# Performance work log

Hardware: AMD Instinct MI355X
Metric: run time of the kernel (lower is better)

Reference implementation:

```python
import jax, jax.numpy as jnp
import numpy as np

N = 100000   # nodes
E = 800000   # edges (avg degree 8)
IN_DIM = 384
HID = 256
BN_EPS = 1e-5


def setup_inputs() -> dict:
    key = jax.random.key(0)
    ks = jax.random.split(key, 12)
    x = jax.random.normal(ks[0], (N, IN_DIM), dtype=jnp.float32)
    edge_index = jax.random.randint(ks[1], (2, E), 0, N, dtype=jnp.int32)
    # GCNConv params (glorot-ish scaling)
    W1 = jax.random.normal(ks[2], (IN_DIM, HID), dtype=jnp.float32) * (1.0 / np.sqrt(IN_DIM))
    b1 = jnp.zeros((HID,), jnp.float32)
    W2 = jax.random.normal(ks[3], (HID, HID), dtype=jnp.float32) * (1.0 / np.sqrt(HID))
    b2 = jnp.zeros((HID,), jnp.float32)
    # BatchNorm affine params
    g1 = jnp.ones((HID,), jnp.float32)
    be1 = jnp.zeros((HID,), jnp.float32)
    g2 = jnp.ones((HID,), jnp.float32)
    be2 = jnp.zeros((HID,), jnp.float32)
    return {"x": x, "edge_index": edge_index, "W1": W1, "b1": b1, "g1": g1,
            "be1": be1, "W2": W2, "b2": b2, "g2": g2, "be2": be2}


def _gcn_conv(x, W, b, src, dst):
    """PyG GCNConv: self-loops + symmetric normalization D^-1/2 A D^-1/2."""
    h = x @ W                                             # [N, H]
    deg = jnp.zeros((x.shape[0],), h.dtype).at[dst].add(1.0) + 1.0  # in-deg + self loop
    dinv = jax.lax.rsqrt(deg)                             # [N]
    coef = dinv[src] * dinv[dst]                          # [E]
    agg = jnp.zeros_like(h).at[dst].add(h[src] * coef[:, None])     # scatter-add messages
    agg = agg + h * (1.0 / deg)[:, None]                  # self-loop term (norm = 1/deg)
    return agg + b


def _batchnorm(h, gamma, beta):
    # training-mode BN over node dim, biased variance (matches torch normalization)
    mu = jnp.mean(h, axis=0)
    var = jnp.mean(jnp.square(h - mu), axis=0)
    return gamma * (h - mu) * jax.lax.rsqrt(var + BN_EPS) + beta


def reference(x, edge_index, W1, b1, g1, be1, W2, b2, g2, be2):
    src, dst = edge_index[0], edge_index[1]
    h = _gcn_conv(x, W1, b1, src, dst)
    h = jax.nn.relu(_batchnorm(h, g1, be1))
    # dropout: eval mode -> identity
    h = _gcn_conv(h, W2, b2, src, dst)
    h = jax.nn.relu(_batchnorm(h, g2, be2))
    return h
```

## Files before the change

kernel.cpp:

```cpp
#include <hip/hip_runtime.h>
#include <hip/hip_bf16.h>

#define NN  100000
#define NE  800000
#define KIN 384
#define HID 256
#define BN_EPS 1e-5f

typedef __attribute__((ext_vector_type(4))) float floatx4;
typedef __attribute__((ext_vector_type(8))) short short8;

__device__ __forceinline__ unsigned short f2b(float f) {
    union { float f; unsigned int u; } v; v.f = f;
    unsigned int r = v.u + 0x7fffu + ((v.u >> 16) & 1u);
    return (unsigned short)(r >> 16);
}
__device__ __forceinline__ float b2f(unsigned short h) {
    union { unsigned int u; float f; } v; v.u = ((unsigned int)h) << 16;
    return v.f;
}

__device__ __forceinline__ void gload_lds16(const void* g, void* l) {
    __builtin_amdgcn_global_load_lds(
        (const __attribute__((address_space(1))) void*)g,
        (__attribute__((address_space(3))) void*)l, 16, 0, 0);
}

__global__ __launch_bounds__(256) void k_prep0(
    const float* __restrict__ W1, unsigned short* __restrict__ W1t,
    const float* __restrict__ W2, unsigned short* __restrict__ W2t,
    const int* __restrict__ dst, int* __restrict__ deg)
{
    const int b = blockIdx.x;
    if (b < KIN) {
        W1t[(size_t)threadIdx.x * KIN + b] = f2b(W1[(size_t)b * HID + threadIdx.x]);
    } else if (b < KIN + HID) {
        const int k2 = b - KIN;
        W2t[(size_t)threadIdx.x * HID + k2] = f2b(W2[(size_t)k2 * HID + threadIdx.x]);
    } else {
        const int i = (b - KIN - HID) * 256 + threadIdx.x;
        if (i < NE) atomicAdd(deg + dst[i], 1);
    }
}

__device__ __forceinline__ int block_incl_scan(int v, int* lds) {
    lds[threadIdx.x] = v; __syncthreads();
    #pragma unroll
    for (int off = 1; off < 256; off <<= 1) {
        int t = lds[threadIdx.x];
        int a = (threadIdx.x >= off) ? lds[threadIdx.x - off] : 0;
        __syncthreads();
        lds[threadIdx.x] = t + a;
        __syncthreads();
    }
    return lds[threadIdx.x];
}

__global__ __launch_bounds__(256) void k_scan1(const int* __restrict__ deg,
                                               int* __restrict__ bsum,
                                               float* __restrict__ dinv) {
    __shared__ int lds[256];
    int i = blockIdx.x * 256 + threadIdx.x;
    int v = (i < NN) ? deg[i] : 0;
    if (i < NN) dinv[i] = rsqrtf((float)(v + 1));
    int incl = block_incl_scan(v, lds);
    if (threadIdx.x == 255) bsum[blockIdx.x] = incl;
}

__global__ __launch_bounds__(512) void k_scan2(const int* __restrict__ bsum,
                                               int* __restrict__ boff, int nb,
                                               int* __restrict__ rowptr) {
    __shared__ int lds[512];
    int v = (threadIdx.x < nb) ? bsum[threadIdx.x] : 0;
    lds[threadIdx.x] = v; __syncthreads();
    #pragma unroll
    for (int off = 1; off < 512; off <<= 1) {
        int t = lds[threadIdx.x];
        int a = (threadIdx.x >= off) ? lds[threadIdx.x - off] : 0;
        __syncthreads();
        lds[threadIdx.x] = t + a;
        __syncthreads();
    }
    if (threadIdx.x < nb) boff[threadIdx.x] = lds[threadIdx.x] - v;
    if (threadIdx.x == 0) rowptr[NN] = NE;
}

__global__ __launch_bounds__(256) void k_scan3(const int* __restrict__ deg,
                                               const int* __restrict__ boff,
                                               int* __restrict__ rowptr) {
    __shared__ int lds[256];
    int i = blockIdx.x * 256 + threadIdx.x;
    int v = (i < NN) ? deg[i] : 0;
    int incl = block_incl_scan(v, lds);
    if (i < NN) rowptr[i] = incl - v + boff[blockIdx.x];
}

__global__ __launch_bounds__(256) void k_fill(
    const int* __restrict__ src, const int* __restrict__ dst,
    const float* __restrict__ dinv, const int* __restrict__ rowptr,
    int* __restrict__ cursor, int2* __restrict__ epk)
{
    int e = blockIdx.x * 256 + threadIdx.x;
    if (e < NE) {
        const int d = dst[e], s = src[e];
        const int pos = rowptr[d] + atomicAdd(cursor + d, 1);
        int2 rec; rec.x = s; rec.y = __float_as_int(dinv[s]);
        epk[pos] = rec;
    }
}

template<int K, int MODE, int ABF16>
__global__ __launch_bounds__(512) void k_gemm(
    const void* __restrict__ Av, const unsigned short* __restrict__ Bt,
    unsigned short* __restrict__ C,
    const float* __restrict__ bnacc, const float* __restrict__ g,
    const float* __restrict__ be, int M)
{
    constexpr int BM = 128, BK = 32, LDA = 40, LDB = 32;
    __shared__ __align__(16) unsigned short As[BM * LDA];
    __shared__ __align__(16) unsigned short Bs[HID * LDB];
    __shared__ float s_sc[HID], s_bi[HID];
    const int tid = threadIdx.x;
    const int lane = tid & 63;
    const int wid  = tid >> 6;
    const int wm = wid & 1, wn = wid >> 1;
    const int l15 = lane & 15, lq = lane >> 4;
    const int row0 = blockIdx.x * BM;

    if (MODE) {
        if (tid < HID) {
            const float inv_n = 1.f / (float)NN;
            const float mu  = bnacc[tid] * inv_n;
            const float var = bnacc[HID + tid] * inv_n - mu * mu;
            const float s   = g[tid] * rsqrtf(var + BN_EPS);
            s_sc[tid] = s;
            s_bi[tid] = be[tid] - s * mu;
        }
        __syncthreads();
    }

    floatx4 acc[4][4] = {};

    const int ar  = tid >> 3;
    const int ak  = (tid & 7) * 4;
    const int ar2 = tid >> 2;
    const int ak2 = (tid & 3) * 8;
    const int lofs = (wid << 11) + lane * 16;
    int brow[2], bcol[2];
    #pragma unroll
    for (int r = 0; r < 2; ++r) {
        const int la = lofs + (r << 10);
        brow[r] = la >> 6;
        bcol[r] = (la & 63) >> 1;
    }

    float4 apf0, apf1;
    short8 apf2 = {};
    if (ABF16) {
        const unsigned short* A = (const unsigned short*)Av;
        const int grow = row0 + ar2;
        if (grow < M) apf2 = *(const short8*)(A + (size_t)grow * K + ak2);
    } else {
        const float* A = (const float*)Av;
        const int g0 = row0 + ar, g1 = row0 + 64 + ar;
        apf0 = (g0 < M) ? *(const float4*)(A + (size_t)g0 * K + ak) : make_float4(0.f,0.f,0.f,0.f);
        apf1 = (g1 < M) ? *(const float4*)(A + (size_t)g1 * K + ak) : make_float4(0.f,0.f,0.f,0.f);
    }

    for (int k0 = 0; k0 < K; k0 += BK) {
        #pragma unroll
        for (int r = 0; r < 2; ++r)
            gload_lds16(Bt + (size_t)brow[r] * K + k0 + bcol[r],
                        (char*)Bs + lofs + (r << 10));

        if (ABF16) {
            float x[8];
            #pragma unroll
            for (int t = 0; t < 8; ++t) x[t] = b2f((unsigned short)apf2[t]);
            if (MODE) {
                float4 s0 = *(const float4*)(s_sc + k0 + ak2);
                float4 s1 = *(const float4*)(s_sc + k0 + ak2 + 4);
                float4 b0 = *(const float4*)(s_bi + k0 + ak2);
                float4 b1 = *(const float4*)(s_bi + k0 + ak2 + 4);
                x[0] = fmaxf(x[0] * s0.x + b0.x, 0.f);
                x[1] = fmaxf(x[1] * s0.y + b0.y, 0.f);
                x[2] = fmaxf(x[2] * s0.z + b0.z, 0.f);
                x[3] = fmaxf(x[3] * s0.w + b0.w, 0.f);
                x[4] = fmaxf(x[4] * s1.x + b1.x, 0.f);
                x[5] = fmaxf(x[5] * s1.y + b1.y, 0.f);
                x[6] = fmaxf(x[6] * s1.z + b1.z, 0.f);
                x[7] = fmaxf(x[7] * s1.w + b1.w, 0.f);
            }
            short8 o;
            #pragma unroll
            for (int t = 0; t < 8; ++t) o[t] = (short)f2b(x[t]);
            *(short8*)(As + ar2 * LDA + ak2) = o;
        } else {
            ushort4 o0, o1;
            o0.x = f2b(apf0.x); o0.y = f2b(apf0.y); o0.z = f2b(apf0.z); o0.w = f2b(apf0.w);
            o1.x = f2b(apf1.x); o1.y = f2b(apf1.y); o1.z = f2b(apf1.z); o1.w = f2b(apf1.w);
            *(ushort4*)(As + ar * LDA + ak) = o0;
            *(ushort4*)(As + (64 + ar) * LDA + ak) = o1;
        }

        const int kn = k0 + BK;
        if (kn < K) {
            if (ABF16) {
                const unsigned short* A = (const unsigned short*)Av;
                const int grow = row0 + ar2;
                apf2 = {};
                if (grow < M) apf2 = *(const short8*)(A + (size_t)grow * K + kn + ak2);
            } else {
                const float* A = (const float*)Av;
                const int g0 = row0 + ar, g1 = row0 + 64 + ar;
                apf0 = (g0 < M) ? *(const float4*)(A + (size_t)g0 * K + kn + ak) : make_float4(0.f,0.f,0.f,0.f);
                apf1 = (g1 < M) ? *(const float4*)(A + (size_t)g1 * K + kn + ak) : make_float4(0.f,0.f,0.f,0.f);
            }
        }

        __syncthreads();

        short8 af[4], bf[4];
        #pragma unroll
        for (int i = 0; i < 4; ++i)
            af[i] = *(const short8*)(As + (wm * 64 + i * 16 + l15) * LDA + lq * 8);
        #pragma unroll
        for (int j = 0; j < 4; ++j)
            bf[j] = *(const short8*)(Bs + (wn * 64 + j * 16 + l15) * LDB + lq * 8);
        #pragma unroll
        for (int i = 0; i < 4; ++i)
            #pragma unroll
            for (int j = 0; j < 4; ++j)
                acc[i][j] = __builtin_amdgcn_mfma_f32_16x16x32_bf16(af[i], bf[j], acc[i][j], 0, 0, 0);
        __syncthreads();
    }

    #pragma unroll
    for (int i = 0; i < 4; ++i) {
        #pragma unroll
        for (int r = 0; r < 4; ++r) {
            const int m = row0 + wm * 64 + i * 16 + lq * 4 + r;
            if (m < M) {
                #pragma unroll
                for (int j = 0; j < 4; ++j) {
                    const int c = wn * 64 + j * 16 + l15;
                    C[(size_t)m * HID + c] = f2b(acc[i][j][r]);
                }
            }
        }
    }
}

__global__ __launch_bounds__(256) void k_gather(
    const unsigned short* __restrict__ H, const int2* __restrict__ epk,
    const int* __restrict__ rowptr, const float* __restrict__ dinv,
    unsigned short* __restrict__ AGGb, float* __restrict__ bn_acc)
{
    __shared__ float ls[512];
    const int tid = threadIdx.x, lane = tid & 63, w = tid >> 6;
    const int half = lane >> 5;
    const int l32  = lane & 31;
    const int c0   = l32 * 8;
    float s[8] = {}, q[8] = {};

    for (int n = blockIdx.x * 4 + w; n < NN; n += gridDim.x * 4) {
        const int beg = rowptr[n], end = rowptr[n + 1];
        const float di = dinv[n];
        float a[8] = {};
        int j = beg;
        for (; j + 8 <= end; j += 8) {
            int2 e[4]; short8 h[4];
            #pragma unroll
            for (int t = 0; t < 4; ++t) e[t] = epk[j + half + 2 * t];
            #pragma unroll
            for (int t = 0; t < 4; ++t)
                h[t] = *(const short8*)(H + (size_t)e[t].x * HID + c0);
            #pragma unroll
            for (int t = 0; t < 4; ++t) {
                const float cf = __int_as_float(e[t].y) * di;
                #pragma unroll
                for (int u = 0; u < 8; ++u)
                    a[u] += b2f((unsigned short)h[t][u]) * cf;
            }
        }
        for (; j + 2 <= end; j += 2) {
            const int2 e = epk[j + half];
            const float cf = __int_as_float(e.y) * di;
            const short8 h = *(const short8*)(H + (size_t)e.x * HID + c0);
            #pragma unroll
            for (int u = 0; u < 8; ++u)
                a[u] += b2f((unsigned short)h[u]) * cf;
        }
        if (j < end && half == 0) {
            const int2 e = epk[j];
            const float cf = __int_as_float(e.y) * di;
            const short8 h = *(const short8*)(H + (size_t)e.x * HID + c0);
            #pragma unroll
            for (int u = 0; u < 8; ++u)
                a[u] += b2f((unsigned short)h[u]) * cf;
        }
        if (half == 1) {
            const float cs = di * di;
            const short8 h = *(const short8*)(H + (size_t)n * HID + c0);
            #pragma unroll
            for (int u = 0; u < 8; ++u)
                a[u] += b2f((unsigned short)h[u]) * cs;
        }
        #pragma unroll
        for (int u = 0; u < 8; ++u)
            a[u] += __shfl_xor(a[u], 32);
        if (half == 0) {
            short8 o;
            #pragma unroll
            for (int u = 0; u < 8; ++u) o[u] = (short)f2b(a[u]);
            *(short8*)(AGGb + (size_t)n * HID + c0) = o;
            #pragma unroll
            for (int u = 0; u < 8; ++u) { s[u] += a[u]; q[u] += a[u] * a[u]; }
        }
    }

    ls[tid] = 0.f; ls[tid + 256] = 0.f;
    __syncthreads();
    if (half == 0) {
        #pragma unroll
        for (int u = 0; u < 8; ++u) {
            atomicAdd(&ls[c0 + u], s[u]);
            atomicAdd(&ls[256 + c0 + u], q[u]);
        }
    }
    __syncthreads();
    atomicAdd(bn_acc + tid, ls[tid]);
    atomicAdd(bn_acc + 256 + tid, ls[tid + 256]);
}

__global__ __launch_bounds__(256) void k_apply(
    const unsigned short* __restrict__ AGGb, const float* __restrict__ bnacc,
    const float* __restrict__ g, const float* __restrict__ be,
    float* __restrict__ out)
{
    const int gid = blockIdx.x * 256 + threadIdx.x;
    if (gid < NN * (HID / 4)) {
        const int c4 = (gid & 63) * 4;
        float sc[4], bi[4];
        const float inv_n = 1.f / (float)NN;
        #pragma unroll
        for (int u = 0; u < 4; ++u) {
            const int c = c4 + u;
            const float mu  = bnacc[c] * inv_n;
            const float var = bnacc[HID + c] * inv_n - mu * mu;
            const float sv  = g[c] * rsqrtf(var + BN_EPS);
            sc[u] = sv; bi[u] = be[c] - sv * mu;
        }
        ushort4 v = *(const ushort4*)(AGGb + (size_t)gid * 4);
        float4 o;
        o.x = fmaxf(b2f(v.x) * sc[0] + bi[0], 0.f);
        o.y = fmaxf(b2f(v.y) * sc[1] + bi[1], 0.f);
        o.z = fmaxf(b2f(v.z) * sc[2] + bi[2], 0.f);
        o.w = fmaxf(b2f(v.w) * sc[3] + bi[3], 0.f);
        *(float4*)(out + (size_t)gid * 4) = o;
    }
}

extern "C" void kernel_launch(void* const* d_in, const int* in_sizes, int n_in,
                              void* d_out, int out_size, void* d_ws, size_t ws_size,
                              hipStream_t stream)
{
    const float* x   = (const float*)d_in[0];
    const int*   ei  = (const int*)d_in[1];
    const float* W1  = (const float*)d_in[2];
    const float* g1  = (const float*)d_in[4];
    const float* be1 = (const float*)d_in[5];
    const float* W2  = (const float*)d_in[6];
    const float* g2  = (const float*)d_in[8];
    const float* be2 = (const float*)d_in[9];
    float* out = (float*)d_out;
    const int* srcp = ei;
    const int* dstp = ei + NE;

    constexpr int NB = (NN + 255) / 256;

    char* p = (char*)d_ws;
    int*            deg    = (int*)p;             p += (size_t)NN * 4;
    int*            cursor = (int*)p;             p += (size_t)NN * 4;
    float*          bn1    = (float*)p;           p += 512 * 4;
    float*          bn2    = (float*)p;           p += 512 * 4;
    const size_t zbytes = (size_t)NN * 8 + 4096;
    unsigned short* AGGb   = (unsigned short*)p;  p += (size_t)NN * HID * 2;
    unsigned short* H      = (unsigned short*)p;  p += (size_t)NN * HID * 2;
    float*          dinv   = (float*)p;           p += (size_t)NN * 4;
    int*            rowptr = (int*)p;             p += (size_t)(NN + 1) * 4;
    int2*           epk    = (int2*)p;            p += (size_t)NE * 8;
    int*            bsum   = (int*)p;             p += 512 * 4;
    int*            boff   = (int*)p;             p += 512 * 4;
    unsigned short* W1t    = (unsigned short*)p;  p += (size_t)KIN * HID * 2;
    unsigned short* W2t    = (unsigned short*)p;  p += (size_t)HID * HID * 2;

    hipMemsetAsync(deg, 0, zbytes, stream);

    k_prep0<<<KIN + HID + (NE + 255) / 256, 256, 0, stream>>>(W1, W1t, W2, W2t, dstp, deg);

    k_scan1<<<NB, 256, 0, stream>>>(deg, bsum, dinv);
    k_scan2<<<1, 512, 0, stream>>>(bsum, boff, NB, rowptr);
    k_scan3<<<NB, 256, 0, stream>>>(deg, boff, rowptr);
    k_fill<<<(NE + 255) / 256, 256, 0, stream>>>(srcp, dstp, dinv, rowptr, cursor, epk);

    const int ggrid = (NN + 127) / 128;

    k_gemm<KIN, 0, 0><<<ggrid, 512, 0, stream>>>(x, W1t, H, nullptr, nullptr, nullptr, NN);
    k_gather<<<2560, 256, 0, stream>>>(H, epk, rowptr, dinv, AGGb, bn1);

    k_gemm<HID, 1, 1><<<ggrid, 512, 0, stream>>>(AGGb, W2t, H, bn1, g1, be1, NN);
    k_gather<<<2560, 256, 0, stream>>>(H, epk, rowptr, dinv, AGGb, bn2);
    k_apply<<<(NN * (HID / 4) + 255) / 256, 256, 0, stream>>>(AGGb, bn2, g2, be2, out);
}
```

Measured before the change: 699.4 us.

## Merge scan kernels, shrink edge records to indices, retune gather and apply

The scan2 and scan3 kernels are merged: each block now sums the preceding block totals itself, which removes one launch. The scan also initialises the cursor to rowptr, so the cursor memset and the rowptr read in fill go away. Edge records shrink from (src, dinv) pairs to plain src indices, so the gather looks up dinv[src] itself. Gather gets launch bounds with an occupancy hint and a smaller grid, and the gather loop no longer batches its four loads before using them, which may lose memory-level parallelism. The final BN-apply kernel is widened to 8 elements per thread.

```diff
diff --git a/kernel.cpp b/kernel.cpp
--- a/kernel.cpp
+++ b/kernel.cpp
@@ -67,45 +67,41 @@
     if (threadIdx.x == 255) bsum[blockIdx.x] = incl;
 }
 
-__global__ __launch_bounds__(512) void k_scan2(const int* __restrict__ bsum,
-                                               int* __restrict__ boff, int nb,
-                                               int* __restrict__ rowptr) {
-    __shared__ int lds[512];
-    int v = (threadIdx.x < nb) ? bsum[threadIdx.x] : 0;
-    lds[threadIdx.x] = v; __syncthreads();
+__global__ __launch_bounds__(256) void k_scan3(const int* __restrict__ deg,
+                                               const int* __restrict__ bsum,
+                                               int* __restrict__ rowptr,
+                                               int* __restrict__ cursor) {
+    __shared__ int lds[256];
+    const int bid = blockIdx.x;
+    int part = 0;
+    for (int i = threadIdx.x; i < bid; i += 256) part += bsum[i];
+    lds[threadIdx.x] = part; __syncthreads();
     #pragma unroll
-    for (int off = 1; off < 512; off <<= 1) {
-        int t = lds[threadIdx.x];
-        int a = (threadIdx.x >= off) ? lds[threadIdx.x - off] : 0;
-        __syncthreads();
-        lds[threadIdx.x] = t + a;
-        __syncthreads();
-    }
-    if (threadIdx.x < nb) boff[threadIdx.x] = lds[threadIdx.x] - v;
-    if (threadIdx.x == 0) rowptr[NN] = NE;
-}
-
-__global__ __launch_bounds__(256) void k_scan3(const int* __restrict__ deg,
-                                               const int* __restrict__ boff,
-                                               int* __restrict__ rowptr) {
-    __shared__ int lds[256];
-    int i = blockIdx.x * 256 + threadIdx.x;
-    int v = (i < NN) ? deg[i] : 0;
-    int incl = block_incl_scan(v, lds);
-    if (i < NN) rowptr[i] = incl - v + boff[blockIdx.x];
+    for (int off = 128; off > 0; off >>= 1) {
+        if (threadIdx.x < off) lds[threadIdx.x] += lds[threadIdx.x + off];
+        __syncthreads();
+    }
+    const int boff = lds[0];
+    __syncthreads();
+    const int i = bid * 256 + threadIdx.x;
+    const int v = (i < NN) ? deg[i] : 0;
+    const int incl = block_incl_scan(v, lds);
+    if (i < NN) {
+        const int rp = incl - v + boff;
+        rowptr[i] = rp;
+        cursor[i] = rp;
+    }
+    if (bid == 0 && threadIdx.x == 0) rowptr[NN] = NE;
 }
 
 __global__ __launch_bounds__(256) void k_fill(
     const int* __restrict__ src, const int* __restrict__ dst,
-    const float* __restrict__ dinv, const int* __restrict__ rowptr,
-    int* __restrict__ cursor, int2* __restrict__ epk)
+    int* __restrict__ cursor, int* __restrict__ eidx)
 {
     int e = blockIdx.x * 256 + threadIdx.x;
     if (e < NE) {
-        const int d = dst[e], s = src[e];
-        const int pos = rowptr[d] + atomicAdd(cursor + d, 1);
-        int2 rec; rec.x = s; rec.y = __float_as_int(dinv[s]);
-        epk[pos] = rec;
+        const int pos = atomicAdd(cursor + dst[e], 1);
+        eidx[pos] = src[e];
     }
 }
 
@@ -251,8 +247,8 @@
     }
 }
 
-__global__ __launch_bounds__(256) void k_gather(
-    const unsigned short* __restrict__ H, const int2* __restrict__ epk,
+__global__ __launch_bounds__(256, 6) void k_gather(
+    const unsigned short* __restrict__ H, const int* __restrict__ eidx,
     const int* __restrict__ rowptr, const float* __restrict__ dinv,
     unsigned short* __restrict__ AGGb, float* __restrict__ bn_acc)
 {
@@ -269,32 +265,28 @@
         float a[8] = {};
         int j = beg;
         for (; j + 8 <= end; j += 8) {
-            int2 e[4]; short8 h[4];
-            #pragma unroll
-            for (int t = 0; t < 4; ++t) e[t] = epk[j + half + 2 * t];
-            #pragma unroll
-            for (int t = 0; t < 4; ++t)
-                h[t] = *(const short8*)(H + (size_t)e[t].x * HID + c0);
             #pragma unroll
             for (int t = 0; t < 4; ++t) {
-                const float cf = __int_as_float(e[t].y) * di;
+                const int sidx = eidx[j + half + 2 * t];
+                const float cf = dinv[sidx] * di;
+                const short8 h = *(const short8*)(H + (size_t)sidx * HID + c0);
                 #pragma unroll
                 for (int u = 0; u < 8; ++u)
-                    a[u] += b2f((unsigned short)h[t][u]) * cf;
+                    a[u] += b2f((unsigned short)h[u]) * cf;
             }
         }
         for (; j + 2 <= end; j += 2) {
-            const int2 e = epk[j + half];
-            const float cf = __int_as_float(e.y) * di;
-            const short8 h = *(const short8*)(H + (size_t)e.x * HID + c0);
+            const int sidx = eidx[j + half];
+            const float cf = dinv[sidx] * di;
+            const short8 h = *(const short8*)(H + (size_t)sidx * HID + c0);
             #pragma unroll
             for (int u = 0; u < 8; ++u)
                 a[u] += b2f((unsigned short)h[u]) * cf;
         }
         if (j < end && half == 0) {
-            const int2 e = epk[j];
-            const float cf = __int_as_float(e.y) * di;
-            const short8 h = *(const short8*)(H + (size_t)e.x * HID + c0);
+            const int sidx = eidx[j];
+            const float cf = dinv[sidx] * di;
+            const short8 h = *(const short8*)(H + (size_t)sidx * HID + c0);
             #pragma unroll
             for (int u = 0; u < 8; ++u)
                 a[u] += b2f((unsigned short)h[u]) * cf;
@@ -339,25 +331,22 @@
     float* __restrict__ out)
 {
     const int gid = blockIdx.x * 256 + threadIdx.x;
-    if (gid < NN * (HID / 4)) {
-        const int c4 = (gid & 63) * 4;
-        float sc[4], bi[4];
+    if (gid < NN * (HID / 8)) {
+        const int c8 = (gid & 31) * 8;
         const float inv_n = 1.f / (float)NN;
-        #pragma unroll
-        for (int u = 0; u < 4; ++u) {
-            const int c = c4 + u;
+        short8 v = *(const short8*)(AGGb + (size_t)gid * 8);
+        float o[8];
+        #pragma unroll
+        for (int u = 0; u < 8; ++u) {
+            const int c = c8 + u;
             const float mu  = bnacc[c] * inv_n;
             const float var = bnacc[HID + c] * inv_n - mu * mu;
             const float sv  = g[c] * rsqrtf(var + BN_EPS);
-            sc[u] = sv; bi[u] = be[c] - sv * mu;
-        }
-        ushort4 v = *(const ushort4*)(AGGb + (size_t)gid * 4);
-        float4 o;
-        o.x = fmaxf(b2f(v.x) * sc[0] + bi[0], 0.f);
-        o.y = fmaxf(b2f(v.y) * sc[1] + bi[1], 0.f);
-        o.z = fmaxf(b2f(v.z) * sc[2] + bi[2], 0.f);
-        o.w = fmaxf(b2f(v.w) * sc[3] + bi[3], 0.f);
-        *(float4*)(out + (size_t)gid * 4) = o;
+            o[u] = fmaxf(b2f((unsigned short)v[u]) * sv + (be[c] - sv * mu), 0.f);
+        }
+        float* op = out + (size_t)gid * 8;
+        *(float4*)(op)     = make_float4(o[0], o[1], o[2], o[3]);
+        *(float4*)(op + 4) = make_float4(o[4], o[5], o[6], o[7]);
     }
 }
 
@@ -381,17 +370,16 @@
 
     char* p = (char*)d_ws;
     int*            deg    = (int*)p;             p += (size_t)NN * 4;
-    int*            cursor = (int*)p;             p += (size_t)NN * 4;
     float*          bn1    = (float*)p;           p += 512 * 4;
     float*          bn2    = (float*)p;           p += 512 * 4;
-    const size_t zbytes = (size_t)NN * 8 + 4096;
+    const size_t zbytes = (size_t)NN * 4 + 4096;
+    int*            cursor = (int*)p;             p += (size_t)NN * 4;
     unsigned short* AGGb   = (unsigned short*)p;  p += (size_t)NN * HID * 2;
     unsigned short* H      = (unsigned short*)p;  p += (size_t)NN * HID * 2;
     float*          dinv   = (float*)p;           p += (size_t)NN * 4;
     int*            rowptr = (int*)p;             p += (size_t)(NN + 1) * 4;
-    int2*           epk    = (int2*)p;            p += (size_t)NE * 8;
+    int*            eidx   = (int*)p;             p += (size_t)NE * 4;
     int*            bsum   = (int*)p;             p += 512 * 4;
-    int*            boff   = (int*)p;             p += 512 * 4;
     unsigned short* W1t    = (unsigned short*)p;  p += (size_t)KIN * HID * 2;
     unsigned short* W2t    = (unsigned short*)p;  p += (size_t)HID * HID * 2;
 
@@ -400,16 +388,15 @@
     k_prep0<<<KIN + HID + (NE + 255) / 256, 256, 0, stream>>>(W1, W1t, W2, W2t, dstp, deg);
 
     k_scan1<<<NB, 256, 0, stream>>>(deg, bsum, dinv);
-    k_scan2<<<1, 512, 0, stream>>>(bsum, boff, NB, rowptr);
-    k_scan3<<<NB, 256, 0, stream>>>(deg, boff, rowptr);
-    k_fill<<<(NE + 255) / 256, 256, 0, stream>>>(srcp, dstp, dinv, rowptr, cursor, epk);
+    k_scan3<<<NB, 256, 0, stream>>>(deg, bsum, rowptr, cursor);
+    k_fill<<<(NE + 255) / 256, 256, 0, stream>>>(srcp, dstp, cursor, eidx);
 
     const int ggrid = (NN + 127) / 128;
 
     k_gemm<KIN, 0, 0><<<ggrid, 512, 0, stream>>>(x, W1t, H, nullptr, nullptr, nullptr, NN);
-    k_gather<<<2560, 256, 0, stream>>>(H, epk, rowptr, dinv, AGGb, bn1);
+    k_gather<<<1536, 256, 0, stream>>>(H, eidx, rowptr, dinv, AGGb, bn1);
 
     k_gemm<HID, 1, 1><<<ggrid, 512, 0, stream>>>(AGGb, W2t, H, bn1, g1, be1, NN);
-    k_gather<<<2560, 256, 0, stream>>>(H, epk, rowptr, dinv, AGGb, bn2);
-    k_apply<<<(NN * (HID / 4) + 255) / 256, 256, 0, stream>>>(AGGb, bn2, g2, be2, out);
-}
+    k_gather<<<1536, 256, 0, stream>>>(H, eidx, rowptr, dinv, AGGb, bn2);
+    k_apply<<<(NN * (HID / 8) + 255) / 256, 256, 0, stream>>>(AGGb, bn2, g2, be2, out);
+}
```

New measurement: 660.4 us. -5.6%, faster.
